# Optimization experiments

Hardware: AMD Instinct MI355X
Metric: run time of the kernel (lower is better)

The kernel has to match this reference:

```python
import jax, jax.numpy as jnp
import numpy as np

T, B, H, EMB, EVO, A = 700, 32, 800, 32, 21, 60
DIN = EMB + EVO            # 53 = embedding + evolutionary profile
RNN_OUT = 2 * H + DIN      # 1653 = bi-LSTM output + skip connection

BOND_LENGTHS = jnp.array([145.801, 152.326, 132.868], jnp.float32)
BOND_ANGLES = jnp.array([2.124, 1.941, 2.028], jnp.float32)
INIT_MAT = jnp.array([[-np.sqrt(0.5), np.sqrt(1.5), 0.0],
                      [-np.sqrt(2.0), 0.0, 0.0],
                      [0.0, 0.0, 0.0]], jnp.float32)


def setup_inputs():
    key = jax.random.key(0)
    ks = jax.random.split(key, 12)
    s = 0.03  # ~ pytorch LSTM uniform(-1/sqrt(H), 1/sqrt(H)) scale

    def lstm_params(k, d):
        k1, k2, k3 = jax.random.split(k, 3)
        return (jax.random.normal(k1, (4 * H, d)) * s,
                jax.random.normal(k2, (4 * H, H)) * s,
                jax.random.normal(k3, (4 * H,)) * s)  # b = b_ih + b_hh fused

    Wih0f, Whh0f, b0f = lstm_params(ks[0], DIN)
    Wih0b, Whh0b, b0b = lstm_params(ks[1], DIN)
    Wih1f, Whh1f, b1f = lstm_params(ks[2], 2 * H)
    Wih1b, Whh1b, b1b = lstm_params(ks[3], 2 * H)
    emb = jax.random.normal(ks[4], (21, EMB)) * s
    emb = emb.at[0].set(0.0)  # padding_idx=0
    fcW = jax.random.normal(ks[5], (A, RNN_OUT)) * s
    fcb = jax.random.normal(ks[6], (A,)) * s
    alphabet = jnp.pi * jnp.tanh(jax.random.normal(ks[7], (A, 3)))  # angularize
    primary = jax.random.randint(ks[8], (T, B), 0, 21)
    evolutionary = jax.random.normal(ks[9], (T, B, EVO))
    return {"primary": primary, "evolutionary": evolutionary, "seq_length": T,
            "emb": emb,
            "Wih0f": Wih0f, "Whh0f": Whh0f, "b0f": b0f,
            "Wih0b": Wih0b, "Whh0b": Whh0b, "b0b": b0b,
            "Wih1f": Wih1f, "Whh1f": Whh1f, "b1f": b1f,
            "Wih1b": Wih1b, "Whh1b": Whh1b, "b1b": b1b,
            "fcW": fcW, "fcb": fcb, "alphabet": alphabet}


def lstm_dir(xs, Wih, Whh, b, reverse):
    """One direction of an LSTM over xs [T, B, D] -> [T, B, H] (PyTorch gate order i,f,g,o)."""
    if reverse:
        xs = xs[::-1]
    xg = jnp.einsum('tbd,gd->tbg', xs, Wih) + b  # precompute input projection

    def step(carry, g_t):
        h, c = carry
        g = g_t + h @ Whh.T
        i, f, gg, o = jnp.split(g, 4, axis=-1)
        c = jax.nn.sigmoid(f) * c + jax.nn.sigmoid(i) * jnp.tanh(gg)
        h = jax.nn.sigmoid(o) * jnp.tanh(c)
        return (h, c), h

    z = jnp.zeros((xs.shape[1], Whh.shape[1]), xs.dtype)
    _, hs = jax.lax.scan(step, (z, z), xg)
    return hs[::-1] if reverse else hs


def dihedral_to_point(dih):
    """dih [T, B, 3] -> backbone points in local frames [3T, B, 3]."""
    rct = BOND_LENGTHS * jnp.cos(jnp.pi - BOND_ANGLES)
    rst = BOND_LENGTHS * jnp.sin(jnp.pi - BOND_ANGLES)
    px = jnp.broadcast_to(rct, dih.shape)
    pts = jnp.stack([px, jnp.cos(dih) * rst, jnp.sin(dih) * rst], axis=-1)  # [T,B,3,3]
    t, b = dih.shape[0], dih.shape[1]
    return pts.transpose(0, 2, 1, 3).reshape(3 * t, b, 3)


def point_to_coordinate(pts):
    """Sequential NeRF extension: pts [3T, B, 3] -> coords [3T, B, 3]."""
    b_sz = pts.shape[1]
    a = jnp.broadcast_to(INIT_MAT[0], (b_sz, 3))
    b = jnp.broadcast_to(INIT_MAT[1], (b_sz, 3))
    c = jnp.broadcast_to(INIT_MAT[2], (b_sz, 3))

    def norm(v):
        return v / jnp.sqrt(jnp.sum(v * v, axis=-1, keepdims=True) + 1e-12)

    def step(carry, p):
        a, b, c = carry
        bc = norm(c - b)
        n = norm(jnp.cross(b - a, bc))
        coord = c + p[:, 0:1] * bc + p[:, 1:2] * jnp.cross(n, bc) + p[:, 2:3] * n
        return (b, c, coord), coord

    _, coords = jax.lax.scan(step, (a, b, c), pts)
    return coords


def reference(primary, evolutionary, seq_length, emb,
              Wih0f, Whh0f, b0f, Wih0b, Whh0b, b0b,
              Wih1f, Whh1f, b1f, Wih1b, Whh1b, b1b,
              fcW, fcb, alphabet):
    # seq_length == T for all sequences, so packing is identity.
    x = jnp.concatenate([emb[primary], evolutionary], axis=-1)  # [T,B,53]
    h0 = jnp.concatenate([lstm_dir(x, Wih0f, Whh0f, b0f, False),
                          lstm_dir(x, Wih0b, Whh0b, b0b, True)], axis=-1)   # [T,B,1600]
    h1 = jnp.concatenate([lstm_dir(h0, Wih1f, Whh1f, b1f, False),
                          lstm_dir(h0, Wih1b, Whh1b, b1b, True)], axis=-1)  # [T,B,1600]
    out = jnp.concatenate([h1, x], axis=-1)  # skip connection -> [T,B,1653]
    logits = jnp.einsum('tbd,ad->tba', out, fcW) + fcb  # [T,B,60]
    probs = jax.nn.softmax(logits, axis=-1)  # alphabet_temperature = 1.0
    dih = jnp.arctan2(probs @ jnp.sin(alphabet), probs @ jnp.cos(alphabet))  # [T,B,3]
    return point_to_coordinate(dihedral_to_point(dih))  # [3T, B, 3]
```

## Files before the change

### kernel.cpp

```cpp
#include <hip/hip_runtime.h>
#include <hip/hip_bf16.h>
#include <math.h>


typedef unsigned int u32;
typedef unsigned long long u64;
typedef __bf16 bf16x8 __attribute__((ext_vector_type(8)));
typedef float  f32x4  __attribute__((ext_vector_type(4)));

#define TT 700
#define BT 32
#define HROW 1664
#define CH 50
#define NCH (TT / CH)
#define SLOT ((size_t)2 * CH * 3200 * 32)
#define LDS_L0 (108 * 512 + 102400)
#define LDS_L1 (100 * 512 + 102400)

__device__ __forceinline__ f32x4 mfma16(bf16x8 a, bf16x8 b, f32x4 c) {
  return __builtin_amdgcn_mfma_f32_16x16x32_bf16(a, b, c, 0, 0, 0);
}
__device__ __forceinline__ float sigf(float x) { return 1.f / (1.f + __expf(-x)); }

#define ALOAD(p)    __hip_atomic_load((p), __ATOMIC_RELAXED, __HIP_MEMORY_SCOPE_AGENT)
#define ASTORE(p,v) __hip_atomic_store((p), (v), __ATOMIC_RELAXED, __HIP_MEMORY_SCOPE_AGENT)

__device__ __forceinline__ void lds_barrier() {
  asm volatile("s_waitcnt lgkmcnt(0)" ::: "memory");
  __builtin_amdgcn_s_barrier();
}

__device__ __forceinline__ bf16x8 cvt8(f32x4 a, f32x4 b) {
  bf16x8 r;
  r[0] = (__bf16)a[0]; r[1] = (__bf16)a[1]; r[2] = (__bf16)a[2]; r[3] = (__bf16)a[3];
  r[4] = (__bf16)b[0]; r[5] = (__bf16)b[1]; r[6] = (__bf16)b[2]; r[7] = (__bf16)b[3];
  return r;
}

__global__ void pack_wx0_kernel(const float* Wih0f, const float* Wih0b, __bf16* wx0) {
  int idx = blockIdx.x * 256 + threadIdx.x;
  if (idx >= 2 * 3200 * 64) return;
  int d = idx / (3200 * 64);
  int r = (idx / 64) % 3200;
  int k = idx % 64;
  const float* W = d ? Wih0b : Wih0f;
  wx0[idx] = (k < 53) ? (__bf16)W[(size_t)r * 53 + k] : (__bf16)0.f;
}

__global__ void pack_fc_kernel(const float* fcW, __bf16* wfc) {
  int idx = blockIdx.x * 256 + threadIdx.x;
  if (idx >= 64 * 1664) return;
  int a = idx / 1664, k = idx % 1664;
  __bf16 v = (__bf16)0.f;
  if (a < 60 && k < 1653) v = (__bf16)fcW[(size_t)a * 1653 + k];
  wfc[idx] = v;
}

__global__ void xpad_kernel(const int* primary, const float* evo,
                            const float* emb, __bf16* xpad) {
  int idx = blockIdx.x * 256 + threadIdx.x;
  int t = idx >> 11;
  int b = (idx >> 6) & 31;
  int k = idx & 63;
  __bf16 v = (__bf16)0.f;
  if (k < 32)      v = (__bf16)emb[primary[t * 32 + b] * 32 + k];
  else if (k < 53) v = (__bf16)evo[((size_t)t * 32 + b) * 21 + (k - 32)];
  xpad[idx] = v;
}

__global__ void small_init_kernel(__bf16* zerobuf, u32* flags,
                                  float* sinA, float* cosA, const float* alpha) {
  int idx = blockIdx.x * 256 + threadIdx.x;
  if (idx < 32 * HROW) zerobuf[idx] = (__bf16)0.f;
  if (idx < 11392) flags[idx] = 0u;
  int j = idx - 32 * HROW;
  if (j >= 0 && j < 192) {
    if (j < 180) {
      float v = alpha[j];
      sinA[j] = sinf(v);
      cosA[j] = cosf(v);
    } else { sinA[j] = 0.f; cosA[j] = 0.f; }
  }
}

__device__ __forceinline__ void wait_lines(u32* flags, int base, int count,
                                           unsigned gen) {
  const int tid = threadIdx.x;
  if (tid < 64) {
    int spin = 0;
    for (;;) {
      bool ok = true;
      for (int j = tid; j < count; j += 64)
        ok = ok && (ALOAD(flags + (size_t)(base + j) * 32) >= gen);
      if (__popcll(__ballot(ok)) == 64) break;
      if (++spin > 24) __builtin_amdgcn_s_sleep(1);
    }
  }
  __syncthreads();
}

__device__ __forceinline__ void rec_barrier(u32* flags, unsigned gen,
                                            int base, int count) {
  asm volatile("s_waitcnt vmcnt(0)" ::: "memory");
  __syncthreads();
  if (threadIdx.x == 0) ASTORE(flags + (size_t)blockIdx.x * 32, gen);
  wait_lines(flags, base, count, gen);
}

struct L0Args {
  const __bf16 *xpad, *wx0, *zero;
  const float *Whh0f, *Whh0b, *b0f, *b0b;
  __bf16* h0;
  u32* flags;
};

__global__ __launch_bounds__(256, 1) void lstm_l0(L0Args A) {
  extern __shared__ __bf16 u2[];
  const int wg = blockIdx.x, d = wg / 50, u0 = (wg % 50) * 16;
  const int tid = threadIdx.x, w = tid >> 6, l = tid & 63;
  const int nidx = l & 15, q = l >> 4, bL = l & 31, gl = l >> 5;
  const int dcol = d * 832;
  const int row = w * 800 + u0 + nidx;
  const float bias_n = (d ? A.b0b : A.b0f)[row];
  const float* wrf = (d ? A.Whh0b : A.Whh0f) + (size_t)row * 800 + q * 8;
  __bf16* wlds = u2 + 108 * 256;
  float* g_lds = (float*)u2;
  const int bb = tid >> 3, up = tid & 7;

#pragma unroll
  for (int sl = 0; sl < 25; ++sl) {
    f32x4 wa = *(const f32x4*)(wrf + sl * 32);
    f32x4 wb = *(const f32x4*)(wrf + sl * 32 + 4);
    *(bf16x8*)(wlds + ((size_t)(w * 25 + sl) * 64 + l) * 8) = cvt8(wa, wb);
  }
  const __bf16* wx_row = A.wx0 + (size_t)d * 3200 * 64 + (size_t)row * 64 + q * 8;
  bf16x8 wx_r0 = *(const bf16x8*)wx_row;
  bf16x8 wx_r1 = *(const bf16x8*)(wx_row + 32);
  __syncthreads();

  float cA = 0.f, cB = 0.f;
#pragma unroll 1
  for (int s = 0; s < TT; ++s) {
    const int tt = d ? (TT - 1 - s) : s;
    const __bf16* hprev =
        (s == 0) ? A.zero : (A.h0 + (size_t)(d ? tt + 1 : tt - 1) * (BT * HROW));

    bf16x8 hreg[13];
    const __bf16* hsrc = hprev + (size_t)bL * HROW + dcol;
#pragma unroll
    for (int i = 0; i < 12; ++i)
      hreg[i] = *(const bf16x8*)(hsrc + (i * 8 + w * 2 + gl) * 8);
    if (w < 2) hreg[12] = *(const bf16x8*)(hsrc + (96 + w * 2 + gl) * 8);
    bf16x8 xv = *(const bf16x8*)(A.xpad + ((size_t)tt * BT + bL) * 64 + (tid >> 5) * 8);

#pragma unroll
    for (int i = 0; i < 12; ++i)
      *(bf16x8*)(u2 + (size_t)(i * 8 + w * 2 + gl) * 256 + bL * 8) = hreg[i];
    if (w < 2)
      *(bf16x8*)(u2 + (size_t)(96 + w * 2 + gl) * 256 + bL * 8) = hreg[12];
    *(bf16x8*)(u2 + (size_t)(100 + (tid >> 5)) * 256 + bL * 8) = xv;
    __syncthreads();

    f32x4 acc0 = {0.f, 0.f, 0.f, 0.f}, acc1 = {0.f, 0.f, 0.f, 0.f};
#pragma unroll
    for (int sl = 0; sl < 27; ++sl) {
      bf16x8 bfr;
      if (sl < 25)
        bfr = *(const bf16x8*)(wlds + ((size_t)(w * 25 + sl) * 64 + l) * 8);
      else
        bfr = (sl == 25) ? wx_r0 : wx_r1;
      const __bf16* ab = u2 + (size_t)(sl * 4 + q) * 256 + nidx * 8;
      bf16x8 a0 = *(const bf16x8*)ab;
      bf16x8 a1 = *(const bf16x8*)(ab + 128);
      acc0 = mfma16(a0, bfr, acc0);
      acc1 = mfma16(a1, bfr, acc1);
    }
    __syncthreads();

#pragma unroll
    for (int r = 0; r < 4; ++r) {
      g_lds[w * 512 + (q * 4 + r) * 16 + nidx]      = acc0[r] + bias_n;
      g_lds[w * 512 + (16 + q * 4 + r) * 16 + nidx] = acc1[r] + bias_n;
    }
    __syncthreads();

    {
      const int uA = 2 * up, uB = uA + 1;
      float iA = g_lds[0 * 512 + bb * 16 + uA], fA = g_lds[1 * 512 + bb * 16 + uA];
      float gA = g_lds[2 * 512 + bb * 16 + uA], oA = g_lds[3 * 512 + bb * 16 + uA];
      cA = sigf(fA) * cA + sigf(iA) * tanhf(gA);
      float hA = sigf(oA) * tanhf(cA);
      float iB = g_lds[0 * 512 + bb * 16 + uB], fB = g_lds[1 * 512 + bb * 16 + uB];
      float gB = g_lds[2 * 512 + bb * 16 + uB], oB = g_lds[3 * 512 + bb * 16 + uB];
      cB = sigf(fB) * cB + sigf(iB) * tanhf(gB);
      float hB = sigf(oB) * tanhf(cB);
      union { u32 u; __bf16 h2[2]; } pk;
      pk.h2[0] = (__bf16)hA;
      pk.h2[1] = (__bf16)hB;
      ASTORE((u32*)(A.h0 + ((size_t)tt * BT + bb) * HROW + dcol + u0 + uA), pk.u);
    }

    if (s < TT - 1) rec_barrier(A.flags, (unsigned)(s + 1), d * 50, 50);
  }
}

struct L1Args {
  const __bf16 *h0, *zero;
  const float *Whh1f, *Whh1b, *Wih1f, *Wih1b, *b1f, *b1b;
  __bf16 *h1, *xg;
  u32* flags;
};

__global__ __launch_bounds__(256, 1) void lstm_l1(L1Args A) {
  extern __shared__ __bf16 u2[];
  const int tid = threadIdx.x, w = tid >> 6, l = tid & 63;
  const int nidx = l & 15, q = l >> 4, bL = l & 31, gl = l >> 5;
  __bf16* wlds = u2 + 100 * 256;

  if (blockIdx.x < 100) {
    const int wg = blockIdx.x, d = wg / 50, u0 = (wg % 50) * 16;
    const int dcol = d * 832;
    const int row = w * 800 + u0 + nidx;
    float* g_lds = (float*)u2;
    const int bb = tid >> 3, up = tid & 7;
    {
      const float* wrf = (d ? A.Whh1b : A.Whh1f) + (size_t)row * 800 + q * 8;
#pragma unroll
      for (int sl = 0; sl < 25; ++sl) {
        f32x4 wa = *(const f32x4*)(wrf + sl * 32);
        f32x4 wb = *(const f32x4*)(wrf + sl * 32 + 4);
        *(bf16x8*)(wlds + ((size_t)(w * 25 + sl) * 64 + l) * 8) = cvt8(wa, wb);
      }
    }
    __syncthreads();
    float cA = 0.f, cB = 0.f;

    for (int k = 0; k < NCH; ++k) {
      wait_lines(A.flags, 100, 156, (unsigned)(k + 1));
      const __bf16* buf = A.xg + (size_t)(k & 1) * SLOT;
      const u64* xga0 = (const u64*)(buf + ((size_t)(d * CH) * 3200 + row) * 32 + q * 4);
      u64 x0 = ALOAD(xga0);
      u64 x1 = ALOAD(xga0 + 4);
#pragma unroll 1
      for (int si = 0; si < CH; ++si) {
        const int s = k * CH + si;
        const int tt = d ? (TT - 1 - s) : s;
        const __bf16* hprev =
            (s == 0) ? A.zero
                     : (A.h1 + (size_t)(d ? tt + 1 : tt - 1) * (BT * HROW));

        u64 cx0 = x0, cx1 = x1;
        if (si + 1 < CH) {
          const u64* xgn = (const u64*)(buf +
              ((size_t)(d * CH + si + 1) * 3200 + row) * 32 + q * 4);
          x0 = ALOAD(xgn);
          x1 = ALOAD(xgn + 4);
        }

        bf16x8 hreg[13];
        const __bf16* hsrc = hprev + (size_t)bL * HROW + dcol;
#pragma unroll
        for (int i = 0; i < 12; ++i)
          hreg[i] = *(const bf16x8*)(hsrc + (i * 8 + w * 2 + gl) * 8);
        if (w < 2) hreg[12] = *(const bf16x8*)(hsrc + (96 + w * 2 + gl) * 8);

        union { u64 u; __bf16 h[4]; } ux0, ux1;
        ux0.u = cx0; ux1.u = cx1;
        f32x4 acc0 = {(float)ux0.h[0], (float)ux0.h[1],
                      (float)ux0.h[2], (float)ux0.h[3]};
        f32x4 acc1 = {(float)ux1.h[0], (float)ux1.h[1],
                      (float)ux1.h[2], (float)ux1.h[3]};

#pragma unroll
        for (int i = 0; i < 12; ++i)
          *(bf16x8*)(u2 + (size_t)(i * 8 + w * 2 + gl) * 256 + bL * 8) = hreg[i];
        if (w < 2)
          *(bf16x8*)(u2 + (size_t)(96 + w * 2 + gl) * 256 + bL * 8) = hreg[12];
        lds_barrier();

#pragma unroll
        for (int sl = 0; sl < 25; ++sl) {
          bf16x8 bfr = *(const bf16x8*)(wlds + ((size_t)(w * 25 + sl) * 64 + l) * 8);
          const __bf16* ab = u2 + (size_t)(sl * 4 + q) * 256 + nidx * 8;
          bf16x8 a0 = *(const bf16x8*)ab;
          bf16x8 a1 = *(const bf16x8*)(ab + 128);
          acc0 = mfma16(a0, bfr, acc0);
          acc1 = mfma16(a1, bfr, acc1);
        }
        lds_barrier();

#pragma unroll
        for (int r = 0; r < 4; ++r) {
          g_lds[w * 512 + (q * 4 + r) * 16 + nidx]      = acc0[r];
          g_lds[w * 512 + (16 + q * 4 + r) * 16 + nidx] = acc1[r];
        }
        lds_barrier();

        {
          const int uA = 2 * up, uB = uA + 1;
          float iA = g_lds[0 * 512 + bb * 16 + uA], fA = g_lds[1 * 512 + bb * 16 + uA];
          float gA = g_lds[2 * 512 + bb * 16 + uA], oA = g_lds[3 * 512 + bb * 16 + uA];
          cA = sigf(fA) * cA + sigf(iA) * tanhf(gA);
          float hA = sigf(oA) * tanhf(cA);
          float iB = g_lds[0 * 512 + bb * 16 + uB], fB = g_lds[1 * 512 + bb * 16 + uB];
          float gB = g_lds[2 * 512 + bb * 16 + uB], oB = g_lds[3 * 512 + bb * 16 + uB];
          cB = sigf(fB) * cB + sigf(iB) * tanhf(gB);
          float hB = sigf(oB) * tanhf(cB);
          union { u32 u; __bf16 h2[2]; } pk;
          pk.h2[0] = (__bf16)hA;
          pk.h2[1] = (__bf16)hB;
          ASTORE((u32*)(A.h1 + ((size_t)tt * BT + bb) * HROW + dcol + u0 + uA), pk.u);
        }

        if (s < TT - 1) rec_barrier(A.flags, (unsigned)(s + 1), 0 + d * 50, 50);
      }
    }
  } else {
    const int g = blockIdx.x - 100;
    const int u_begin = (g * 400) / 156;
    const int u_end   = ((g + 1) * 400) / 156;
    const int nslots  = (u_end - u_begin) * 50;
    const int rh = w >> 1, bh = w & 1;

    bf16x8 pre[13];
    f32x4 acc = {0.f, 0.f, 0.f, 0.f};
    int cur_tl = -1;
    float bn = 0.f;
    int rr = 0;

    for (int k = 0; k < NCH; ++k) {
      if (k >= 2) wait_lines(A.flags, 0, 100, (unsigned)((k - 1) * CH));
      __bf16* buf = A.xg + (size_t)(k & 1) * SLOT;

      {
        const int th0 = u_begin & 1;
        const int dir0 = (u_begin >> 1) / 100;
        const int tloc0 = th0 * 25;
        const int t0 = dir0 ? (TT - 1 - k * CH - tloc0) : (k * CH + tloc0);
        const __bf16* hs = A.h0 + ((size_t)t0 * BT + bL) * HROW;
#pragma unroll
        for (int i = 0; i < 12; ++i)
          pre[i] = *(const bf16x8*)(hs + (i * 8 + w * 2 + gl) * 8);
        if (w < 2) pre[12] = *(const bf16x8*)(hs + (96 + w * 2 + gl) * 8);
      }

#pragma unroll 1
      for (int s = 0; s < nslots; ++s) {
        const int u = u_begin + s / 50;
        const int r = s % 50;
        const int tl = u >> 1, th = u & 1;
        const int tloc = th * 25 + (r >> 1);
        const int pass = r & 1;
        const int dir = tl / 100, rt = tl % 100;
        const int rbase = rt * 32;

        if (tl != cur_tl) {
          cur_tl = tl;
          const float* W = dir ? A.Wih1b : A.Wih1f;
          __syncthreads();
          for (int i = w * 25; i < w * 25 + 25; ++i) {
            const int rhh = i / 50, sl = i % 50;
            const int rrr = rbase + rhh * 16 + nidx;
            const float* wp = W + (size_t)rrr * 1600 + sl * 32 + q * 8;
            f32x4 wa = *(const f32x4*)wp;
            f32x4 wb = *(const f32x4*)(wp + 4);
            *(bf16x8*)(wlds + ((size_t)i * 64 + l) * 8) = cvt8(wa, wb);
          }
          __syncthreads();
          rr = rbase + rh * 16 + nidx;
          bn = (dir ? A.b1b : A.b1f)[rr];
        }

#pragma unroll
        for (int i = 0; i < 12; ++i)
          *(bf16x8*)(u2 + (size_t)(i * 8 + w * 2 + gl) * 256 + bL * 8) = pre[i];
        if (w < 2)
          *(bf16x8*)(u2 + (size_t)(96 + w * 2 + gl) * 256 + bL * 8) = pre[12];
        lds_barrier();

        if (s + 1 < nslots) {
          const int s2 = s + 1;
          const int un = u_begin + s2 / 50;
          const int r2 = s2 % 50;
          const int thn = un & 1;
          const int tlocn = thn * 25 + (r2 >> 1);
          const int passn = r2 & 1;
          const int dirn = (un >> 1) / 100;
          const int tn = dirn ? (TT - 1 - k * CH - tlocn) : (k * CH + tlocn);
          const __bf16* hs = A.h0 + ((size_t)tn * BT + bL) * HROW + passn * 832;
#pragma unroll
          for (int i = 0; i < 12; ++i)
            pre[i] = *(const bf16x8*)(hs + (i * 8 + w * 2 + gl) * 8);
          if (w < 2) pre[12] = *(const bf16x8*)(hs + (96 + w * 2 + gl) * 8);
        }
        __builtin_amdgcn_sched_barrier(0);

        if (pass == 0) acc = f32x4{0.f, 0.f, 0.f, 0.f};
#pragma unroll
        for (int sl = 0; sl < 25; ++sl) {
          bf16x8 b = *(const bf16x8*)(wlds +
              ((size_t)(rh * 50 + pass * 25 + sl) * 64 + l) * 8);
          bf16x8 a = *(const bf16x8*)(u2 +
              (size_t)(sl * 4 + q) * 256 + (bh * 16 + nidx) * 8);
          acc = mfma16(a, b, acc);
        }
        lds_barrier();

        if (pass == 1) {
          union { u64 u; __bf16 h[4]; } pv;
#pragma unroll
          for (int r2 = 0; r2 < 4; ++r2) pv.h[r2] = (__bf16)(acc[r2] + bn);
          ASTORE((u64*)(buf + ((size_t)(dir * CH + tloc) * 3200 + rr) * 32 +
                        bh * 16 + q * 4), pv.u);
        }
      }
      asm volatile("s_waitcnt vmcnt(0)" ::: "memory");
      __syncthreads();
      if (tid == 0) ASTORE(A.flags + (size_t)(100 + g) * 32, (unsigned)(k + 1));
    }
  }
}

__global__ __launch_bounds__(256) void fc_kernel(
    const __bf16* __restrict__ h1, const __bf16* __restrict__ xpad,
    const __bf16* __restrict__ wfc, const float* __restrict__ fcb,
    const float* __restrict__ sinA, const float* __restrict__ cosA,
    float* __restrict__ pts) {
  __shared__ float lg[32 * 64];
  const int t = blockIdx.x, tid = threadIdx.x;
  const int wave = tid >> 6, lane = tid & 63, nidx = lane & 15, q = lane >> 4;
  const int a_col = wave * 16 + nidx;
  const __bf16* wrow = wfc + (size_t)a_col * 1664 + q * 8;
  const __bf16* h1row = h1 + (size_t)t * BT * HROW;
  const __bf16* xrow  = xpad + (size_t)t * BT * 64;
  f32x4 acc0 = {0.f, 0.f, 0.f, 0.f}, acc1 = {0.f, 0.f, 0.f, 0.f};
#pragma unroll
  for (int sl = 0; sl < 52; ++sl) {
    const int k = sl * 32 + q * 8;
    bf16x8 a0, a1;
    if (sl < 50) {
      const int kp = (sl < 25) ? k : (k + 32);
      a0 = *(const bf16x8*)(h1row + (size_t)nidx * HROW + kp);
      a1 = *(const bf16x8*)(h1row + (size_t)(16 + nidx) * HROW + kp);
    } else {
      a0 = *(const bf16x8*)(xrow + nidx * 64 + (k - 1600));
      a1 = *(const bf16x8*)(xrow + (16 + nidx) * 64 + (k - 1600));
    }
    bf16x8 bfr = *(const bf16x8*)(wrow + sl * 32);
    acc0 = mfma16(a0, bfr, acc0);
    acc1 = mfma16(a1, bfr, acc1);
  }
  const float bn = (a_col < 60) ? fcb[a_col] : -1e30f;
#pragma unroll
  for (int r = 0; r < 4; ++r) {
    lg[(q * 4 + r) * 64 + a_col]      = acc0[r] + bn;
    lg[(16 + q * 4 + r) * 64 + a_col] = acc1[r] + bn;
  }
  __syncthreads();

  const int b = tid >> 3, j = tid & 7;
  float v[8];
  float m = -1e30f;
#pragma unroll
  for (int k2 = 0; k2 < 8; ++k2) {
    v[k2] = lg[b * 64 + j + 8 * k2];
    m = fmaxf(m, v[k2]);
  }
  m = fmaxf(m, __shfl_xor(m, 1, 8));
  m = fmaxf(m, __shfl_xor(m, 2, 8));
  m = fmaxf(m, __shfl_xor(m, 4, 8));
  float s = 0.f;
#pragma unroll
  for (int k2 = 0; k2 < 8; ++k2) { v[k2] = __expf(v[k2] - m); s += v[k2]; }
  s += __shfl_xor(s, 1, 8);
  s += __shfl_xor(s, 2, 8);
  s += __shfl_xor(s, 4, 8);
  const float inv = 1.f / s;
  float ps[3] = {0.f, 0.f, 0.f}, pc[3] = {0.f, 0.f, 0.f};
#pragma unroll
  for (int k2 = 0; k2 < 8; ++k2) {
    const int a = j + 8 * k2;
    const float p = v[k2] * inv;
#pragma unroll
    for (int c = 0; c < 3; ++c) {
      ps[c] += p * sinA[a * 3 + c];
      pc[c] += p * cosA[a * 3 + c];
    }
  }
#pragma unroll
  for (int c = 0; c < 3; ++c) {
    ps[c] += __shfl_xor(ps[c], 1, 8);
    ps[c] += __shfl_xor(ps[c], 2, 8);
    ps[c] += __shfl_xor(ps[c], 4, 8);
    pc[c] += __shfl_xor(pc[c], 1, 8);
    pc[c] += __shfl_xor(pc[c], 2, 8);
    pc[c] += __shfl_xor(pc[c], 4, 8);
  }
  if (j == 0) {
    const float BL[3] = {145.801f, 152.326f, 132.868f};
    const float BA[3] = {2.124f, 1.941f, 2.028f};
#pragma unroll
    for (int c = 0; c < 3; ++c) {
      const float ang = 3.14159265358979323846f - BA[c];
      const float rct = BL[c] * cosf(ang), rst = BL[c] * sinf(ang);
      const float dih = atan2f(ps[c], pc[c]);
      float* o = pts + ((size_t)(3 * t + c) * BT + b) * 3;
      o[0] = rct;
      o[1] = cosf(dih) * rst;
      o[2] = sinf(dih) * rst;
    }
  }
}

__global__ void nerf_kernel(const float* __restrict__ pts, float* __restrict__ out) {
  const int b = threadIdx.x;
  if (b >= 32) return;
  float ax = -0.70710678f, ay = 1.22474487f, az = 0.f;
  float bx = -1.41421356f, by = 0.f, bz = 0.f;
  float cx = 0.f, cy = 0.f, cz = 0.f;
#pragma unroll 4
  for (int i = 0; i < 3 * TT; ++i) {
    const float* p = pts + ((size_t)i * BT + b) * 3;
    const float p0 = p[0], p1 = p[1], p2 = p[2];
    float ux = cx - bx, uy = cy - by, uz = cz - bz;
    const float ri = rsqrtf(ux * ux + uy * uy + uz * uz + 1e-12f);
    ux *= ri; uy *= ri; uz *= ri;
    const float wx = bx - ax, wy = by - ay, wz = bz - az;
    float nx = wy * uz - wz * uy, ny = wz * ux - wx * uz, nz = wx * uy - wy * ux;
    const float rn = rsqrtf(nx * nx + ny * ny + nz * nz + 1e-12f);
    nx *= rn; ny *= rn; nz *= rn;
    const float mx = ny * uz - nz * uy, my = nz * ux - nx * uz, mz = nx * uy - ny * ux;
    const float ox = cx + p0 * ux + p1 * mx + p2 * nx;
    const float oy = cy + p0 * uy + p1 * my + p2 * ny;
    const float oz = cz + p0 * uz + p1 * mz + p2 * nz;
    out[((size_t)i * BT + b) * 3 + 0] = ox;
    out[((size_t)i * BT + b) * 3 + 1] = oy;
    out[((size_t)i * BT + b) * 3 + 2] = oz;
    ax = bx; ay = by; az = bz;
    bx = cx; by = cy; bz = cz;
    cx = ox; cy = oy; cz = oz;
  }
}

extern "C" void kernel_launch(void* const* d_in, const int* in_sizes, int n_in,
                              void* d_out, int out_size, void* d_ws, size_t ws_size,
                              hipStream_t stream) {
  (void)in_sizes; (void)n_in; (void)out_size;
  const int*   primary = (const int*)d_in[0];
  const float* evo     = (const float*)d_in[1];
  const float* emb     = (const float*)d_in[3];
  const float* Wih0f   = (const float*)d_in[4];
  const float* Whh0f   = (const float*)d_in[5];
  const float* b0f     = (const float*)d_in[6];
  const float* Wih0b   = (const float*)d_in[7];
  const float* Whh0b   = (const float*)d_in[8];
  const float* b0b     = (const float*)d_in[9];
  const float* Wih1f   = (const float*)d_in[10];
  const float* Whh1f   = (const float*)d_in[11];
  const float* b1f     = (const float*)d_in[12];
  const float* Wih1b   = (const float*)d_in[13];
  const float* Whh1b   = (const float*)d_in[14];
  const float* b1b     = (const float*)d_in[15];
  const float* fcW     = (const float*)d_in[16];
  const float* fcb     = (const float*)d_in[17];
  const float* alpha   = (const float*)d_in[18];

  char* ws = (char*)d_ws;
  size_t off = 0;
  auto take = [&](size_t n) -> void* {
    void* p = ws + off;
    off += (n + 511) & ~(size_t)511;
    return p;
  };
  __bf16* xpad = (__bf16*)take((size_t)TT * BT * 64 * 2);
  __bf16* zb   = (__bf16*)take((size_t)BT * HROW * 2);
  __bf16* wx0  = (__bf16*)take((size_t)2 * 3200 * 64 * 2);
  __bf16* wfc  = (__bf16*)take((size_t)64 * 1664 * 2);
  float*  sinA = (float*)take(192 * 4);
  float*  cosA = (float*)take(192 * 4);
  float*  pts  = (float*)take((size_t)3 * TT * BT * 3 * 4);
  u32*    flags0 = (u32*)take(11392 * 4);
  u32*    flags1 = flags0 + 3200;
  __bf16* xg   = (__bf16*)take(2 * SLOT * 2);
  __bf16* h0   = (__bf16*)take((size_t)TT * BT * HROW * 2);
  __bf16* h1   = (__bf16*)take((size_t)TT * BT * HROW * 2);
  if (off > ws_size) return;

  static int lds_cfg = 0;
  if (!lds_cfg) {
    hipFuncSetAttribute((const void*)lstm_l0,
                        hipFuncAttributeMaxDynamicSharedMemorySize, LDS_L0);
    hipFuncSetAttribute((const void*)lstm_l1,
                        hipFuncAttributeMaxDynamicSharedMemorySize, LDS_L1);
    lds_cfg = 1;
  }

  pack_wx0_kernel<<<1600, 256, 0, stream>>>(Wih0f, Wih0b, wx0);
  pack_fc_kernel<<<(64 * 1664 + 255) / 256, 256, 0, stream>>>(fcW, wfc);
  xpad_kernel<<<(TT * BT * 64) / 256, 256, 0, stream>>>(primary, evo, emb, xpad);
  small_init_kernel<<<209, 256, 0, stream>>>(zb, flags0, sinA, cosA, alpha);

  L0Args a0;
  a0.xpad = xpad; a0.wx0 = wx0; a0.zero = zb;
  a0.Whh0f = Whh0f; a0.Whh0b = Whh0b; a0.b0f = b0f; a0.b0b = b0b;
  a0.h0 = h0; a0.flags = flags0;
  lstm_l0<<<100, 256, LDS_L0, stream>>>(a0);

  L1Args a1;
  a1.h0 = h0; a1.zero = zb;
  a1.Whh1f = Whh1f; a1.Whh1b = Whh1b;
  a1.Wih1f = Wih1f; a1.Wih1b = Wih1b;
  a1.b1f = b1f; a1.b1b = b1b;
  a1.h1 = h1; a1.xg = xg; a1.flags = flags1;
  lstm_l1<<<256, 256, LDS_L1, stream>>>(a1);

  fc_kernel<<<TT, 256, 0, stream>>>(h1, xpad, wfc, fcb, sinA, cosA, pts);
  nerf_kernel<<<1, 64, 0, stream>>>(pts, (float*)d_out);
}
```

Baseline: 9.024 ms.

## Remap LSTM gate rows so gates are combined in-register via shuffles instead of LDS

Each wave's MFMA output columns are remapped so that the four gates (i,f,g,o) of one hidden unit land in adjacent lanes. Cross-lane xor shuffles then transpose them in registers, replacing the LDS round trip and two block barriers per timestep in both LSTM layers. Neighbouring lanes exchange results once more so they can write packed bf16 pairs to global memory. The per-step serial latency of the recurrence should drop, at the cost of extra shuffle instructions and a more intricate row mapping that must match the weight and bias layout.

After: 9.200 ms. Within noise of the previous version (+2.0%).

```diff
diff --git a/kernel.cpp b/kernel.cpp
--- a/kernel.cpp
+++ b/kernel.cpp
@@ -36,6 +36,20 @@
   r[4] = (__bf16)b[0]; r[5] = (__bf16)b[1]; r[6] = (__bf16)b[2]; r[7] = (__bf16)b[3];
   return r;
 }
+
+#define QUAD_TRANSPOSE(l_, a0, a1, a2, a3, o0, o1, o2, o3)                   \
+  {                                                                          \
+    float s0 = __shfl_xor(a0, 1), s1 = __shfl_xor(a1, 1);                    \
+    float s2 = __shfl_xor(a2, 1), s3 = __shfl_xor(a3, 1);                    \
+    const bool e1 = ((l_) & 1) == 0;                                         \
+    float n0 = e1 ? a0 : s1, n1 = e1 ? s0 : a1;                              \
+    float n2 = e1 ? a2 : s3, n3 = e1 ? s2 : a3;                              \
+    float t0 = __shfl_xor(n0, 2), t1 = __shfl_xor(n1, 2);                    \
+    float t2 = __shfl_xor(n2, 2), t3 = __shfl_xor(n3, 2);                    \
+    const bool e2 = ((l_) & 2) == 0;                                         \
+    o0 = e2 ? n0 : t2; o1 = e2 ? n1 : t3;                                    \
+    o2 = e2 ? t0 : n2; o3 = e2 ? t1 : n3;                                    \
+  }
 
 __global__ void pack_wx0_kernel(const float* Wih0f, const float* Wih0b, __bf16* wx0) {
   int idx = blockIdx.x * 256 + threadIdx.x;
@@ -120,12 +134,10 @@
   const int tid = threadIdx.x, w = tid >> 6, l = tid & 63;
   const int nidx = l & 15, q = l >> 4, bL = l & 31, gl = l >> 5;
   const int dcol = d * 832;
-  const int row = w * 800 + u0 + nidx;
+  const int row = (nidx & 3) * 800 + u0 + 4 * w + (nidx >> 2);
   const float bias_n = (d ? A.b0b : A.b0f)[row];
   const float* wrf = (d ? A.Whh0b : A.Whh0f) + (size_t)row * 800 + q * 8;
   __bf16* wlds = u2 + 108 * 256;
-  float* g_lds = (float*)u2;
-  const int bb = tid >> 3, up = tid & 7;
 
 #pragma unroll
   for (int sl = 0; sl < 25; ++sl) {
@@ -175,29 +187,30 @@
       acc0 = mfma16(a0, bfr, acc0);
       acc1 = mfma16(a1, bfr, acc1);
     }
-    __syncthreads();
-
-#pragma unroll
-    for (int r = 0; r < 4; ++r) {
-      g_lds[w * 512 + (q * 4 + r) * 16 + nidx]      = acc0[r] + bias_n;
-      g_lds[w * 512 + (16 + q * 4 + r) * 16 + nidx] = acc1[r] + bias_n;
-    }
-    __syncthreads();
 
     {
-      const int uA = 2 * up, uB = uA + 1;
-      float iA = g_lds[0 * 512 + bb * 16 + uA], fA = g_lds[1 * 512 + bb * 16 + uA];
-      float gA = g_lds[2 * 512 + bb * 16 + uA], oA = g_lds[3 * 512 + bb * 16 + uA];
+      float a0 = acc0[0] + bias_n, a1 = acc0[1] + bias_n,
+            a2 = acc0[2] + bias_n, a3 = acc0[3] + bias_n;
+      float e0 = acc1[0] + bias_n, e1v = acc1[1] + bias_n,
+            e2v = acc1[2] + bias_n, e3 = acc1[3] + bias_n;
+      float iA, fA, gA, oA, iB, fB, gB, oB;
+      QUAD_TRANSPOSE(l, a0, a1, a2, a3, iA, fA, gA, oA);
+      QUAD_TRANSPOSE(l, e0, e1v, e2v, e3, iB, fB, gB, oB);
       cA = sigf(fA) * cA + sigf(iA) * tanhf(gA);
       float hA = sigf(oA) * tanhf(cA);
-      float iB = g_lds[0 * 512 + bb * 16 + uB], fB = g_lds[1 * 512 + bb * 16 + uB];
-      float gB = g_lds[2 * 512 + bb * 16 + uB], oB = g_lds[3 * 512 + bb * 16 + uB];
       cB = sigf(fB) * cB + sigf(iB) * tanhf(gB);
       float hB = sigf(oB) * tanhf(cB);
-      union { u32 u; __bf16 h2[2]; } pk;
-      pk.h2[0] = (__bf16)hA;
-      pk.h2[1] = (__bf16)hB;
-      ASTORE((u32*)(A.h0 + ((size_t)tt * BT + bb) * HROW + dcol + u0 + uA), pk.u);
+      float hA2 = __shfl_xor(hA, 4);
+      float hB2 = __shfl_xor(hB, 4);
+      if ((l & 4) == 0) {
+        const int bA = q * 4 + (nidx & 3);
+        const int colp = dcol + u0 + 4 * w + (nidx >> 2);
+        union { u32 u; __bf16 h2[2]; } pk;
+        pk.h2[0] = (__bf16)hA; pk.h2[1] = (__bf16)hA2;
+        ASTORE((u32*)(A.h0 + ((size_t)tt * BT + bA) * HROW + colp), pk.u);
+        pk.h2[0] = (__bf16)hB; pk.h2[1] = (__bf16)hB2;
+        ASTORE((u32*)(A.h0 + ((size_t)tt * BT + bA + 16) * HROW + colp), pk.u);
+      }
     }
 
     if (s < TT - 1) rec_barrier(A.flags, (unsigned)(s + 1), d * 50, 50);
@@ -220,9 +233,7 @@
   if (blockIdx.x < 100) {
     const int wg = blockIdx.x, d = wg / 50, u0 = (wg % 50) * 16;
     const int dcol = d * 832;
-    const int row = w * 800 + u0 + nidx;
-    float* g_lds = (float*)u2;
-    const int bb = tid >> 3, up = tid & 7;
+    const int row = (nidx & 3) * 800 + u0 + 4 * w + (nidx >> 2);
     {
       const float* wrf = (d ? A.Whh1b : A.Whh1f) + (size_t)row * 800 + q * 8;
 #pragma unroll
@@ -287,29 +298,28 @@
           acc0 = mfma16(a0, bfr, acc0);
           acc1 = mfma16(a1, bfr, acc1);
         }
-        lds_barrier();
-
-#pragma unroll
-        for (int r = 0; r < 4; ++r) {
-          g_lds[w * 512 + (q * 4 + r) * 16 + nidx]      = acc0[r];
-          g_lds[w * 512 + (16 + q * 4 + r) * 16 + nidx] = acc1[r];
-        }
-        lds_barrier();
 
         {
-          const int uA = 2 * up, uB = uA + 1;
-          float iA = g_lds[0 * 512 + bb * 16 + uA], fA = g_lds[1 * 512 + bb * 16 + uA];
-          float gA = g_lds[2 * 512 + bb * 16 + uA], oA = g_lds[3 * 512 + bb * 16 + uA];
+          float a0 = acc0[0], a1 = acc0[1], a2 = acc0[2], a3 = acc0[3];
+          float e0 = acc1[0], e1v = acc1[1], e2v = acc1[2], e3 = acc1[3];
+          float iA, fA, gA, oA, iB, fB, gB, oB;
+          QUAD_TRANSPOSE(l, a0, a1, a2, a3, iA, fA, gA, oA);
+          QUAD_TRANSPOSE(l, e0, e1v, e2v, e3, iB, fB, gB, oB);
           cA = sigf(fA) * cA + sigf(iA) * tanhf(gA);
           float hA = sigf(oA) * tanhf(cA);
-          float iB = g_lds[0 * 512 + bb * 16 + uB], fB = g_lds[1 * 512 + bb * 16 + uB];
-          float gB = g_lds[2 * 512 + bb * 16 + uB], oB = g_lds[3 * 512 + bb * 16 + uB];
           cB = sigf(fB) * cB + sigf(iB) * tanhf(gB);
           float hB = sigf(oB) * tanhf(cB);
-          union { u32 u; __bf16 h2[2]; } pk;
-          pk.h2[0] = (__bf16)hA;
-          pk.h2[1] = (__bf16)hB;
-          ASTORE((u32*)(A.h1 + ((size_t)tt * BT + bb) * HROW + dcol + u0 + uA), pk.u);
+          float hA2 = __shfl_xor(hA, 4);
+          float hB2 = __shfl_xor(hB, 4);
+          if ((l & 4) == 0) {
+            const int bA = q * 4 + (nidx & 3);
+            const int colp = dcol + u0 + 4 * w + (nidx >> 2);
+            union { u32 u; __bf16 h2[2]; } pk;
+            pk.h2[0] = (__bf16)hA; pk.h2[1] = (__bf16)hA2;
+            ASTORE((u32*)(A.h1 + ((size_t)tt * BT + bA) * HROW + colp), pk.u);
+            pk.h2[0] = (__bf16)hB; pk.h2[1] = (__bf16)hB2;
+            ASTORE((u32*)(A.h1 + ((size_t)tt * BT + bA + 16) * HROW + colp), pk.u);
+          }
         }
 
         if (s < TT - 1) rec_barrier(A.flags, (unsigned)(s + 1), 0 + d * 50, 50);
```
